# Optimization experiments

Hardware: AMD Instinct MI355X
Metric: run time of the kernel (lower is better)

The kernel has to match this reference:

```python
import jax, jax.numpy as jnp
import numpy as np

B, C = 16384, 5000
EPS = 1e-6
NEG_BIG = -1e30  # stand-in for -inf so rows with no positives stay finite


def setup_inputs() -> dict:
    key = jax.random.key(0)
    k1, k2, k3 = jax.random.split(key, 3)
    inp = jax.random.normal(k1, (B, C), dtype=jnp.float32)
    target = jax.random.randint(k2, (B, C), 0, 2, dtype=jnp.int32)
    weights = jax.random.uniform(k3, (B,), dtype=jnp.float32)
    return {"input": inp, "target": target, "weights": weights}


def reference(input, target, weights):
    # loss_ij = target_ij * log(clamp(sigmoid(x_ij), eps, 1-eps))
    logp = jnp.log(jnp.clip(jax.nn.sigmoid(input), EPS, 1.0 - EPS))  # [B, C], all < 0
    t = target.astype(logp.dtype)
    pos = t > 0
    # Original code: for rows with k positives, take max of loss over the positive
    # labels, then abs (entries are negative, so abs == negate). For k == 1 the
    # -sum over the row equals the same thing. Rows with zero positives stay 0.
    masked = jnp.where(pos, logp, NEG_BIG)            # [B, C]
    row_max = jnp.max(masked, axis=1)                 # [B]
    has_pos = jnp.any(pos, axis=1)                    # [B]
    loss1 = jnp.where(has_pos, -row_max, 0.0)         # [B], non-negative
    loss1 = loss1 * weights                           # instance-wise weights
    return jnp.mean(loss1)                            # aggregate='mean'
```

## Files before the change

kernel.cpp:

```cpp
#include <hip/hip_runtime.h>


#define NROWS 16384
#define NCOLS 5000
#define NVEC  (NCOLS / 4)
#define EPSF  1e-6f

__global__ __launch_bounds__(256) void row_loss_kernel(
    const float* __restrict__ inp,
    const int*   __restrict__ tgt,
    const float* __restrict__ w,
    float*       __restrict__ row_loss)
{
    const int row = blockIdx.x;
    const float4* __restrict__ x4 = (const float4*)(inp + (size_t)row * NCOLS);
    const int4*   __restrict__ t4 = (const int4*)(tgt + (size_t)row * NCOLS);

    const float NEG = -3.0e38f;
    float m = NEG;
    for (int i = threadIdx.x; i < NVEC; i += 256) {
        float4 x = x4[i];
        int4   t = t4[i];
        m = fmaxf(m, (t.x > 0) ? x.x : NEG);
        m = fmaxf(m, (t.y > 0) ? x.y : NEG);
        m = fmaxf(m, (t.z > 0) ? x.z : NEG);
        m = fmaxf(m, (t.w > 0) ? x.w : NEG);
    }

    #pragma unroll
    for (int off = 32; off > 0; off >>= 1)
        m = fmaxf(m, __shfl_xor(m, off, 64));

    __shared__ float smax[4];
    const int lane = threadIdx.x & 63;
    const int wid  = threadIdx.x >> 6;
    if (lane == 0) smax[wid] = m;
    __syncthreads();

    if (threadIdx.x == 0) {
        m = fmaxf(fmaxf(smax[0], smax[1]), fmaxf(smax[2], smax[3]));
        float loss = 0.0f;
        if (m > -1.0e38f) {
            float p = 1.0f / (1.0f + expf(-m));
            p = fminf(fmaxf(p, EPSF), 1.0f - EPSF);
            loss = -logf(p) * w[row];
        }
        row_loss[row] = loss;
    }
}

__global__ __launch_bounds__(256) void reduce_mean_kernel(
    const float* __restrict__ row_loss,
    float*       __restrict__ out)
{
    float s = 0.0f;
    for (int i = threadIdx.x; i < NROWS; i += 256)
        s += row_loss[i];

    #pragma unroll
    for (int off = 32; off > 0; off >>= 1)
        s += __shfl_xor(s, off, 64);

    __shared__ float ssum[4];
    const int lane = threadIdx.x & 63;
    const int wid  = threadIdx.x >> 6;
    if (lane == 0) ssum[wid] = s;
    __syncthreads();

    if (threadIdx.x == 0) {
        float tot = ssum[0] + ssum[1] + ssum[2] + ssum[3];
        out[0] = tot / (float)NROWS;
    }
}

extern "C" void kernel_launch(void* const* d_in, const int* in_sizes, int n_in,
                              void* d_out, int out_size, void* d_ws, size_t ws_size,
                              hipStream_t stream) {
    const float* inp = (const float*)d_in[0];
    const int*   tgt = (const int*)d_in[1];
    const float* w   = (const float*)d_in[2];
    float* row_loss  = (float*)d_ws;
    float* out       = (float*)d_out;

    row_loss_kernel<<<NROWS, 256, 0, stream>>>(inp, tgt, w, row_loss);
    reduce_mean_kernel<<<1, 256, 0, stream>>>(row_loss, out);
}
```

Before: 621.6 us.

## Assign rows to waves with batched nontemporal loads and vectorized final reduction

The row kernel now gives each 64-lane wave two whole rows instead of one row per 256-thread block. It loads its data in unrolled batches of five float4/int4 nontemporal loads, so more memory requests are in flight per thread and LDS and __syncthreads are no longer needed. The launch drops to 2048 blocks. The mean reduction uses 1024 threads with float4 loads. The risks are higher register pressure and fewer blocks to hide latency, in exchange for more memory-level parallelism on a bandwidth-bound stream of about 650MB.

```diff
diff --git a/kernel.cpp b/kernel.cpp
--- a/kernel.cpp
+++ b/kernel.cpp
@@ -6,69 +6,93 @@
 #define NVEC  (NCOLS / 4)
 #define EPSF  1e-6f
 
+typedef float fvec4 __attribute__((ext_vector_type(4)));
+typedef int   ivec4 __attribute__((ext_vector_type(4)));
+
 __global__ __launch_bounds__(256) void row_loss_kernel(
     const float* __restrict__ inp,
     const int*   __restrict__ tgt,
     const float* __restrict__ w,
     float*       __restrict__ row_loss)
 {
-    const int row = blockIdx.x;
-    const float4* __restrict__ x4 = (const float4*)(inp + (size_t)row * NCOLS);
-    const int4*   __restrict__ t4 = (const int4*)(tgt + (size_t)row * NCOLS);
-
+    const int lane = threadIdx.x & 63;
+    const int wid  = threadIdx.x >> 6;
+    const int wave_global = blockIdx.x * 4 + wid;
     const float NEG = -3.0e38f;
-    float m = NEG;
-    for (int i = threadIdx.x; i < NVEC; i += 256) {
-        float4 x = x4[i];
-        int4   t = t4[i];
-        m = fmaxf(m, (t.x > 0) ? x.x : NEG);
-        m = fmaxf(m, (t.y > 0) ? x.y : NEG);
-        m = fmaxf(m, (t.z > 0) ? x.z : NEG);
-        m = fmaxf(m, (t.w > 0) ? x.w : NEG);
-    }
 
     #pragma unroll
-    for (int off = 32; off > 0; off >>= 1)
-        m = fmaxf(m, __shfl_xor(m, off, 64));
+    for (int rr = 0; rr < 2; ++rr) {
+        const int row = wave_global * 2 + rr;
+        const fvec4* __restrict__ x4 = (const fvec4*)(inp + (size_t)row * NCOLS);
+        const ivec4* __restrict__ t4 = (const ivec4*)(tgt + (size_t)row * NCOLS);
 
-    __shared__ float smax[4];
-    const int lane = threadIdx.x & 63;
-    const int wid  = threadIdx.x >> 6;
-    if (lane == 0) smax[wid] = m;
-    __syncthreads();
+        float m = NEG;
+        #pragma unroll
+        for (int g = 0; g < 4; ++g) {
+            fvec4 xv[5];
+            ivec4 tv[5];
+            #pragma unroll
+            for (int k = 0; k < 5; ++k) {
+                const int idx = (g * 5 + k) * 64 + lane;
+                if (idx < NVEC) {
+                    xv[k] = __builtin_nontemporal_load(x4 + idx);
+                    tv[k] = __builtin_nontemporal_load(t4 + idx);
+                } else {
+                    xv[k] = (fvec4)0.0f;
+                    tv[k] = (ivec4)0;
+                }
+            }
+            #pragma unroll
+            for (int k = 0; k < 5; ++k) {
+                m = fmaxf(m, (tv[k][0] > 0) ? xv[k][0] : NEG);
+                m = fmaxf(m, (tv[k][1] > 0) ? xv[k][1] : NEG);
+                m = fmaxf(m, (tv[k][2] > 0) ? xv[k][2] : NEG);
+                m = fmaxf(m, (tv[k][3] > 0) ? xv[k][3] : NEG);
+            }
+        }
 
-    if (threadIdx.x == 0) {
-        m = fmaxf(fmaxf(smax[0], smax[1]), fmaxf(smax[2], smax[3]));
-        float loss = 0.0f;
-        if (m > -1.0e38f) {
-            float p = 1.0f / (1.0f + expf(-m));
-            p = fminf(fmaxf(p, EPSF), 1.0f - EPSF);
-            loss = -logf(p) * w[row];
+        #pragma unroll
+        for (int off = 32; off > 0; off >>= 1)
+            m = fmaxf(m, __shfl_xor(m, off, 64));
+
+        if (lane == 0) {
+            float loss = 0.0f;
+            if (m > -1.0e38f) {
+                float p = 1.0f / (1.0f + __expf(-m));
+                p = fminf(fmaxf(p, EPSF), 1.0f - EPSF);
+                loss = -logf(p) * w[row];
+            }
+            row_loss[row] = loss;
         }
-        row_loss[row] = loss;
     }
 }
 
-__global__ __launch_bounds__(256) void reduce_mean_kernel(
+__global__ __launch_bounds__(1024) void reduce_mean_kernel(
     const float* __restrict__ row_loss,
     float*       __restrict__ out)
 {
+    const fvec4* __restrict__ rl4 = (const fvec4*)row_loss;
     float s = 0.0f;
-    for (int i = threadIdx.x; i < NROWS; i += 256)
-        s += row_loss[i];
+    #pragma unroll
+    for (int j = 0; j < 4; ++j) {
+        fvec4 v = rl4[threadIdx.x + j * 1024];
+        s += (v[0] + v[1]) + (v[2] + v[3]);
+    }
 
     #pragma unroll
     for (int off = 32; off > 0; off >>= 1)
         s += __shfl_xor(s, off, 64);
 
-    __shared__ float ssum[4];
+    __shared__ float ssum[16];
     const int lane = threadIdx.x & 63;
     const int wid  = threadIdx.x >> 6;
     if (lane == 0) ssum[wid] = s;
     __syncthreads();
 
     if (threadIdx.x == 0) {
-        float tot = ssum[0] + ssum[1] + ssum[2] + ssum[3];
+        float tot = 0.0f;
+        #pragma unroll
+        for (int i = 0; i < 16; ++i) tot += ssum[i];
         out[0] = tot / (float)NROWS;
     }
 }
@@ -82,6 +106,6 @@
     float* row_loss  = (float*)d_ws;
     float* out       = (float*)d_out;
 
-    row_loss_kernel<<<NROWS, 256, 0, stream>>>(inp, tgt, w, row_loss);
-    reduce_mean_kernel<<<1, 256, 0, stream>>>(row_loss, out);
+    row_loss_kernel<<<2048, 256, 0, stream>>>(inp, tgt, w, row_loss);
+    reduce_mean_kernel<<<1, 1024, 0, stream>>>(row_loss, out);
 }
```

Result: faster. 571.8 us (-8.0%).
